# Kernel optimization log

Measured on AMD Instinct MI355X. Metric: run time of the kernel, lower is better.

## Reference

```python
import jax, jax.numpy as jnp
import numpy as np

HIDDEN = 1024
HEADS = 16
HEAD_DIM = HIDDEN // HEADS  # 64
B, S = 2, 2048


def setup_inputs() -> dict:
    key = jax.random.key(0)
    ks = jax.random.split(key, 12)
    lim_h = 1.0 / np.sqrt(HEAD_DIM)
    lim_o = 1.0 / np.sqrt(HIDDEN)
    u = lambda k, shape, lim: jax.random.uniform(k, shape, jnp.float32, -lim, lim)
    return {
        "query": jax.random.normal(ks[0], (B, S, HIDDEN), jnp.float32),
        "key": jax.random.normal(ks[1], (B, S, HIDDEN), jnp.float32),
        "value": jax.random.normal(ks[2], (B, S, HIDDEN), jnp.float32),
        "mask": jax.random.randint(ks[3], (B, 1, S, S), 0, 2, jnp.int32),
        "Wq": u(ks[4], (HEAD_DIM, HEAD_DIM), lim_h), "bq": u(ks[5], (HEAD_DIM,), lim_h),
        "Wk": u(ks[6], (HEAD_DIM, HEAD_DIM), lim_h), "bk": u(ks[7], (HEAD_DIM,), lim_h),
        "Wv": u(ks[8], (HEAD_DIM, HEAD_DIM), lim_h), "bv": u(ks[9], (HEAD_DIM,), lim_h),
        "Wo": u(ks[10], (HIDDEN, HIDDEN), lim_o), "bo": u(ks[11], (HIDDEN,), lim_o),
    }


def reference(query, key, value, mask, Wq, bq, Wk, bk, Wv, bv, Wo, bo):
    b = query.shape[0]
    # view [B, S, H, D]; per-head linear is SHARED across heads (head_dim x head_dim)
    q = query.reshape(b, -1, HEADS, HEAD_DIM) @ Wq.T + bq
    k = key.reshape(b, -1, HEADS, HEAD_DIM) @ Wk.T + bk
    v = value.reshape(b, -1, HEADS, HEAD_DIM) @ Wv.T + bv
    scores = jnp.einsum('nqhd,nkhd->nhqk', q, k)  # [B, H, Sq, Sk]
    scores = jnp.where(mask == 0, jnp.float32(-1e20), scores)
    # NOTE: original scales by sqrt(hidden_dim), not sqrt(head_dim)
    attn = jax.nn.softmax(scores / np.sqrt(HIDDEN).astype(np.float32), axis=3)
    out = jnp.einsum('nhql,nlhd->nqhd', attn, v).reshape(b, query.shape[1], HIDDEN)
    return out @ Wo.T + bo
```

## Files before the change

kernel.cpp:

```cpp
#include <hip/hip_runtime.h>
#include <hip/hip_bf16.h>

#define NB 2
#define NS 2048
#define NH 16
#define ND 64
#define NHID 1024

#define QSCALE 0.045084220f

typedef __attribute__((ext_vector_type(8))) short bf16x8;
typedef __attribute__((ext_vector_type(4))) short s16x4;
typedef __attribute__((ext_vector_type(4))) float f32x4;

typedef __attribute__((address_space(3))) unsigned int lds_u32;
typedef __attribute__((address_space(1))) unsigned int glb_u32;

__device__ inline void gl_lds16(const void* g, void* l) {
  __builtin_amdgcn_global_load_lds((const glb_u32*)g, (lds_u32*)l, 16, 0, 0);
}

__device__ inline short f2bf(float f) {
  __hip_bfloat16 h = __float2bfloat16(f);
  short s; __builtin_memcpy(&s, &h, 2); return s;
}

__device__ inline float selbit(float e, unsigned long long m) {
  float r;
  asm("v_cndmask_b32 %0, 0, %1, %2" : "=v"(r) : "v"(e), "s"(m));
  return r;
}

__device__ inline bf16x8 cvt8(const float* __restrict__ p) {
  float4 x = *(const float4*)p;
  float4 y = *(const float4*)(p + 4);
  bf16x8 r;
  r[0] = f2bf(x.x); r[1] = f2bf(x.y); r[2] = f2bf(x.z); r[3] = f2bf(x.w);
  r[4] = f2bf(y.x); r[5] = f2bf(y.y); r[6] = f2bf(y.z); r[7] = f2bf(y.w);
  return r;
}

__global__ __launch_bounds__(256) void prep(
    const int* __restrict__ mask, unsigned long long* __restrict__ mp,
    const float* __restrict__ Wq, const float* __restrict__ Wk,
    const float* __restrict__ Wv, const float* __restrict__ Wo,
    short* __restrict__ Wq_b, short* __restrict__ Wk_b,
    short* __restrict__ Wv_b, short* __restrict__ Wo_b)
{
  if (blockIdx.x < 512) {
    int idx = blockIdx.x * 256 + threadIdx.x;
    int lane = threadIdx.x & 63;
    int q4 = lane >> 4;
    int g4 = ((idx >> 6) << 4) | (lane & 15);
    int mt = g4 & 3, kt = (g4 >> 2) & 31, qg = (g4 >> 7) & 127, b = g4 >> 14;
    unsigned long long wq[4] = {0ull, 0ull, 0ull, 0ull};
#pragma unroll
    for (int cc = 0; cc < 4; ++cc) {
      int c2 = q4 * 4 + cc;
      const int4* p = (const int4*)(mask +
          ((size_t)(b * NS + qg * 16 + c2) * NS) + kt * 64 + mt * 16);
#pragma unroll
      for (int qq2 = 0; qq2 < 4; ++qq2) {
        int4 v = p[qq2];
        int sh = qq2 * 16 + c2;
        wq[0] |= (unsigned long long)(v.x != 0) << sh;
        wq[1] |= (unsigned long long)(v.y != 0) << sh;
        wq[2] |= (unsigned long long)(v.z != 0) << sh;
        wq[3] |= (unsigned long long)(v.w != 0) << sh;
      }
    }
#pragma unroll
    for (int r = 0; r < 4; ++r) {
      wq[r] |= __shfl_xor(wq[r], 16);
      wq[r] |= __shfl_xor(wq[r], 32);
    }
    mp[(size_t)g4 * 4 + q4] = wq[q4];
  } else {
    int i = ((blockIdx.x - 512) * 256 + threadIdx.x) * 4;
    const float* src; short* dst; int off; float sc = 1.0f;
    if (i < 1048576)      { src = Wo; dst = Wo_b; off = i; }
    else {
      int j = i - 1048576;
      if (j < 4096)       { src = Wq; dst = Wq_b; off = j; sc = QSCALE; }
      else if (j < 8192)  { src = Wk; dst = Wk_b; off = j - 4096; }
      else                { src = Wv; dst = Wv_b; off = j - 8192; }
    }
    float4 v = *(const float4*)(src + off);
    s16x4 o;
    o[0] = f2bf(v.x * sc); o[1] = f2bf(v.y * sc);
    o[2] = f2bf(v.z * sc); o[3] = f2bf(v.w * sc);
    *(s16x4*)(dst + off) = o;
  }
}

__global__ __launch_bounds__(256) void qkv_proj(
    const float* __restrict__ qin, const float* __restrict__ kin,
    const float* __restrict__ vin,
    const short* __restrict__ Wq_b, const float* __restrict__ bq,
    const short* __restrict__ Wk_b, const float* __restrict__ bk,
    const short* __restrict__ Wv_b, const float* __restrict__ bv,
    short* __restrict__ Qws, short* __restrict__ Kws, short* __restrict__ Vt)
{
  __shared__ __align__(16) short lds[4][16][72];
  const int tid = threadIdx.x;

  if (blockIdx.x < NB * NS / 4) {
    const int w = tid >> 6, lane = tid & 63;
    const int c = lane & 15, qq = lane >> 4;
    const int t = blockIdx.x * 4 + w;
    const int b = t >> 11, s = t & (NS - 1);
    const int aoff = (t * 16 + c) * 64 + qq * 8;
    const int row0 = lane >> 3, inner = lane & 7;

#pragma unroll
    for (int m = 0; m < 2; ++m) {
      const float* X  = (m == 0) ? qin  : kin;
      const short* W  = (m == 0) ? Wq_b : Wk_b;
      const float* bb = (m == 0) ? bq   : bk;
      short* dst      = (m == 0) ? Qws  : Kws;
      const float bsc = (m == 0) ? QSCALE : 1.0f;

      bf16x8 a0 = cvt8(X + aoff);
      bf16x8 a1 = cvt8(X + aoff + 32);

#pragma unroll
      for (int nt = 0; nt < 4; ++nt) {
        f32x4 z = {0.f, 0.f, 0.f, 0.f};
        const short* wp = W + (nt * 16 + c) * 64 + qq * 8;
        bf16x8 b0 = *(const bf16x8*)(wp);
        bf16x8 b1 = *(const bf16x8*)(wp + 32);
        z = __builtin_amdgcn_mfma_f32_16x16x32_bf16(a0, b0, z, 0, 0, 0);
        z = __builtin_amdgcn_mfma_f32_16x16x32_bf16(a1, b1, z, 0, 0, 0);
        float bias = bb[nt * 16 + c] * bsc;
#pragma unroll
        for (int r = 0; r < 4; ++r)
          lds[w][qq * 4 + r][nt * 16 + c] = f2bf(z[r] + bias);
      }

      bf16x8 v0 = *(const bf16x8*)&lds[w][row0][inner * 8];
      bf16x8 v1 = *(const bf16x8*)&lds[w][row0 + 8][inner * 8];
      int bh0 = b * NH + row0, bh1 = b * NH + row0 + 8;
      *(bf16x8*)(dst + (bh0 * NS + s) * 64 + inner * 8) = v0;
      *(bf16x8*)(dst + (bh1 * NS + s) * 64 + inner * 8) = v1;
    }
  } else {
    short (*ldsVT)[72] = (short (*)[72])lds;
    const int bid = blockIdx.x - NB * NS / 4;
    const int g = tid >> 6, lane = tid & 63;
    const int c = lane & 15, qq = lane >> 4;
    const int bh = bid >> 5;
    const int stile = bid & 31;
    const int b = bh >> 4, h = bh & 15;
    const int sb = stile * 64;

    bf16x8 wv[8];
    float bias[4];
#pragma unroll
    for (int nt = 0; nt < 4; ++nt) {
      const short* wp = Wv_b + (nt * 16 + c) * 64 + qq * 8;
      wv[nt * 2]     = *(const bf16x8*)(wp);
      wv[nt * 2 + 1] = *(const bf16x8*)(wp + 32);
      bias[nt] = bv[nt * 16 + c];
    }

    const float* ap = vin + ((size_t)((b * NS + sb + 16 * g + c) * 16 + h)) * 64 + qq * 8;
    bf16x8 a0 = cvt8(ap);
    bf16x8 a1 = cvt8(ap + 32);
#pragma unroll
    for (int nt = 0; nt < 4; ++nt) {
      f32x4 z = {0.f, 0.f, 0.f, 0.f};
      z = __builtin_amdgcn_mfma_f32_16x16x32_bf16(a0, wv[nt * 2], z, 0, 0, 0);
      z = __builtin_amdgcn_mfma_f32_16x16x32_bf16(a1, wv[nt * 2 + 1], z, 0, 0, 0);
      ushort4 u;
      u.x = (unsigned short)f2bf(z[0] + bias[nt]);
      u.y = (unsigned short)f2bf(z[1] + bias[nt]);
      u.z = (unsigned short)f2bf(z[2] + bias[nt]);
      u.w = (unsigned short)f2bf(z[3] + bias[nt]);
      *(ushort4*)&ldsVT[nt * 16 + c][16 * g + qq * 4] = u;
    }
    __syncthreads();

#pragma unroll
    for (int j = 0; j < 2; ++j) {
      int idx = tid + 256 * j;
      int d = idx >> 3, unit = idx & 7;
      bf16x8 o = *(const bf16x8*)&ldsVT[d][unit * 8];
      *(bf16x8*)(Vt + ((size_t)(bh * 64 + d)) * NS + sb + unit * 8) = o;
    }
  }
}

__global__ __launch_bounds__(256, 4) void attn(
    const short* __restrict__ Qws, const short* __restrict__ Kws,
    const short* __restrict__ Vt, const unsigned long long* __restrict__ Mp,
    short* __restrict__ AO)
{
  __shared__ __align__(16) short Ks[2][64][64];
  __shared__ __align__(16) short Vs[2][64][64];
  __shared__ __align__(16) short Ps[4][16][64];

  const int tid = threadIdx.x;
  const int w = tid >> 6, lane = tid & 63;
  const int c = lane & 15, qq = lane >> 4;
  const int bh = blockIdx.x & 31;
  const int qtile = blockIdx.x >> 5;
  const int b = bh >> 4, h = bh & 15;
  const int qbase = qtile * 64 + w * 16;
  const int ca2 = (lane & 7) << 1;

  const short* Qp = Qws + (size_t)bh * (NS * 64);
  const short* Kp = Kws + (size_t)bh * (NS * 64);
  const short* Vp = Vt + (size_t)bh * (64 * NS);

  const int wu = __builtin_amdgcn_readfirstlane(w);
  const unsigned long long* mbase =
      Mp + (size_t)(b * (NS / 16) + qtile * 4 + wu) * ((NS / 64) * 16);

  bf16x8 aq0, aq1;
  {
    const short* qp = Qp + (qbase + c) * 64 + qq * 8;
    aq0 = *(const bf16x8*)(qp);
    aq1 = *(const bf16x8*)(qp + 32);
  }

  float lsum = 0.f;
  f32x4 O[4];
#pragma unroll
  for (int dt = 0; dt < 4; ++dt) { f32x4 z = {0.f, 0.f, 0.f, 0.f}; O[dt] = z; }

  short* Pw = &Ps[w][c][0];

  const int srow = lane >> 3;
  const int sunit = (lane & 7) ^ srow;
  auto stage = [&](int kt, int buf) {
#pragma unroll
    for (int i = 0; i < 2; ++i) {
      int j = w * 2 + i;
      const short* gk = Kp + ((size_t)(kt * 64 + j * 8 + srow)) * 64 + sunit * 8;
      gl_lds16(gk, &Ks[buf][0][0] + j * 512);
      const short* gv = Vp + ((size_t)(j * 8 + srow)) * NS + kt * 64 + sunit * 8;
      gl_lds16(gv, &Vs[buf][0][0] + j * 512);
    }
  };

  stage(0, 0);
  __syncthreads();

  for (int kt = 0; kt < NS / 64; ++kt) {
    const int buf = kt & 1;
    if (kt < NS / 64 - 1) stage(kt + 1, buf ^ 1);

    unsigned long long mw[16];
#pragma unroll
    for (int i = 0; i < 16; ++i) mw[i] = mbase[(size_t)kt * 16 + i];

    f32x4 st[4];
    __builtin_amdgcn_s_setprio(1);
#pragma unroll
    for (int mt = 0; mt < 4; ++mt) {
      const short* kb = &Ks[buf][mt * 16 + c][0];
      bf16x8 ak0 = *(const bf16x8*)(kb + ((qq ^ (c & 7)) << 3));
      bf16x8 ak1 = *(const bf16x8*)(kb + (((4 + qq) ^ (c & 7)) << 3));
      f32x4 z = {0.f, 0.f, 0.f, 0.f};
      z = __builtin_amdgcn_mfma_f32_16x16x32_bf16(ak0, aq0, z, 0, 0, 0);
      z = __builtin_amdgcn_mfma_f32_16x16x32_bf16(ak1, aq1, z, 0, 0, 0);
      st[mt] = z;
    }
    __builtin_amdgcn_s_setprio(0);

#pragma unroll
    for (int mt = 0; mt < 4; ++mt) {
      f32x4 s = st[mt];
      float e0 = selbit(__builtin_amdgcn_exp2f(s[0]), mw[mt * 4 + 0]);
      float e1 = selbit(__builtin_amdgcn_exp2f(s[1]), mw[mt * 4 + 1]);
      float e2 = selbit(__builtin_amdgcn_exp2f(s[2]), mw[mt * 4 + 2]);
      float e3 = selbit(__builtin_amdgcn_exp2f(s[3]), mw[mt * 4 + 3]);
      lsum += (e0 + e1) + (e2 + e3);
      ushort4 u;
      u.x = (unsigned short)f2bf(e0);
      u.y = (unsigned short)f2bf(e1);
      u.z = (unsigned short)f2bf(e2);
      u.w = (unsigned short)f2bf(e3);
      *(ushort4*)&Pw[((mt * 4 + qq) ^ ca2) << 2] = u;
    }

    __builtin_amdgcn_s_setprio(1);
#pragma unroll
    for (int ks = 0; ks < 2; ++ks) {
      bf16x8 pf = *(const bf16x8*)&Pw[((ks * 8 + qq * 2) ^ ca2) << 2];
#pragma unroll
      for (int dt = 0; dt < 4; ++dt) {
        const short* vb = &Vs[buf][dt * 16 + c][0];
        bf16x8 vf = *(const bf16x8*)(vb + ((((ks << 2) + qq) ^ (c & 7)) << 3));
        O[dt] = __builtin_amdgcn_mfma_f32_16x16x32_bf16(vf, pf, O[dt], 0, 0, 0);
      }
    }
    __builtin_amdgcn_s_setprio(0);

    __syncthreads();
  }

  {
    float v = lsum;
    v += __shfl_xor(v, 16);
    v += __shfl_xor(v, 32);
    lsum = 1.0f / fmaxf(v, 1e-30f);
  }

  const int row = qbase + c;
#pragma unroll
  for (int dt = 0; dt < 4; ++dt) {
    ushort4 u;
    u.x = (unsigned short)f2bf(O[dt][0] * lsum);
    u.y = (unsigned short)f2bf(O[dt][1] * lsum);
    u.z = (unsigned short)f2bf(O[dt][2] * lsum);
    u.w = (unsigned short)f2bf(O[dt][3] * lsum);
    *(ushort4*)(AO + ((size_t)(b * NS + row)) * NHID + h * 64 + dt * 16 + qq * 4) = u;
  }
}

__global__ __launch_bounds__(256, 3) void oproj(
    const short* __restrict__ X, const short* __restrict__ Wo_b,
    const float* __restrict__ bo, float* __restrict__ out)
{
  __shared__ __align__(16) short As[2][64][64];
  __shared__ __align__(16) short Bs[2][128][64];
  const int tid = threadIdx.x;
  const int w = tid >> 6, lane = tid & 63;
  const int c = lane & 15, qq = lane >> 4;
  const int rowbase = blockIdx.x * 64;
  const int colbase = blockIdx.y * 128;
  const int mh = w & 1, nh = w >> 1;

  const int srow = lane >> 3;
  const int sunit = (lane & 7) ^ srow;

  auto stage = [&](int kb, int buf) {
#pragma unroll
    for (int i = 0; i < 6; ++i) {
      int t = w * 6 + i;
      if (t < 8) {
        const short* g = X + (size_t)(rowbase + t * 8 + srow) * NHID
                           + kb * 64 + sunit * 8;
        gl_lds16(g, &As[buf][0][0] + t * 512);
      } else {
        int j = t - 8;
        const short* g = Wo_b + (size_t)(colbase + j * 8 + srow) * NHID
                              + kb * 64 + sunit * 8;
        gl_lds16(g, &Bs[buf][0][0] + j * 512);
      }
    }
  };

  f32x4 acc[2][4];
#pragma unroll
  for (int mt = 0; mt < 2; ++mt)
#pragma unroll
    for (int nt = 0; nt < 4; ++nt) { f32x4 z = {0.f, 0.f, 0.f, 0.f}; acc[mt][nt] = z; }

  stage(0, 0);
  __syncthreads();

  for (int kb = 0; kb < NHID / 64; ++kb) {
    const int buf = kb & 1;
    if (kb < NHID / 64 - 1) stage(kb + 1, buf ^ 1);

    bf16x8 af[2][2];
#pragma unroll
    for (int mt = 0; mt < 2; ++mt) {
      const short* ap = &As[buf][mh * 32 + mt * 16 + c][0];
#pragma unroll
      for (int ks = 0; ks < 2; ++ks)
        af[mt][ks] = *(const bf16x8*)(ap + ((((ks << 2) + qq) ^ (c & 7)) << 3));
    }
#pragma unroll
    for (int nt = 0; nt < 4; ++nt) {
      const short* bp = &Bs[buf][nh * 64 + nt * 16 + c][0];
#pragma unroll
      for (int ks = 0; ks < 2; ++ks) {
        bf16x8 bf = *(const bf16x8*)(bp + ((((ks << 2) + qq) ^ (c & 7)) << 3));
#pragma unroll
        for (int mt = 0; mt < 2; ++mt)
          acc[mt][nt] = __builtin_amdgcn_mfma_f32_16x16x32_bf16(af[mt][ks], bf, acc[mt][nt], 0, 0, 0);
      }
    }

    __syncthreads();
  }

#pragma unroll
  for (int nt = 0; nt < 4; ++nt) {
    int col = colbase + nh * 64 + nt * 16 + c;
    float bias = bo[col];
#pragma unroll
    for (int mt = 0; mt < 2; ++mt) {
      int row = rowbase + mh * 32 + mt * 16 + qq * 4;
#pragma unroll
      for (int r = 0; r < 4; ++r)
        out[(size_t)(row + r) * NHID + col] = acc[mt][nt][r] + bias;
    }
  }
}

extern "C" void kernel_launch(void* const* d_in, const int* in_sizes, int n_in,
                              void* d_out, int out_size, void* d_ws, size_t ws_size,
                              hipStream_t stream) {
  const float* qin = (const float*)d_in[0];
  const float* kin = (const float*)d_in[1];
  const float* vin = (const float*)d_in[2];
  const int*  mask = (const int*)d_in[3];
  const float* Wq = (const float*)d_in[4];
  const float* bq = (const float*)d_in[5];
  const float* Wk = (const float*)d_in[6];
  const float* bk = (const float*)d_in[7];
  const float* Wv = (const float*)d_in[8];
  const float* bv = (const float*)d_in[9];
  const float* Wo = (const float*)d_in[10];
  const float* bo = (const float*)d_in[11];
  float* out = (float*)d_out;

  char* ws = (char*)d_ws;
  short* Qws = (short*)(ws);
  short* Kws = (short*)(ws + (size_t)(8 << 20));
  short* Vt  = (short*)(ws + (size_t)(16 << 20));
  short* AO  = (short*)(ws + (size_t)(24 << 20));
  unsigned long long* Mp = (unsigned long long*)(ws + (size_t)(32 << 20));
  short* Wo_b = (short*)(ws + (size_t)(33 << 20));
  short* Wq_b = (short*)(ws + (size_t)(35 << 20));
  short* Wk_b = (short*)(ws + (size_t)(35 << 20) + 8192);
  short* Wv_b = (short*)(ws + (size_t)(35 << 20) + 16384);

  prep<<<1548, 256, 0, stream>>>(mask, Mp, Wq, Wk, Wv, Wo, Wq_b, Wk_b, Wv_b, Wo_b);
  qkv_proj<<<NB * NS / 4 + (NB * NH) * (NS / 64), 256, 0, stream>>>(
      qin, kin, vin, Wq_b, bq, Wk_b, bk, Wv_b, bv, Qws, Kws, Vt);
  attn<<<(NB * NH) * (NS / 64), 256, 0, stream>>>(Qws, Kws, Vt, Mp, AO);
  oproj<<<dim3(64, 8), 256, 0, stream>>>(AO, Wo_b, bo, out);
}
```

Measured before the change: 210.4 us.

## Process two 16-row query tiles per wave in attention kernel

Each wave now handles 32 query rows instead of 16, so the attention block covers 128 queries and the grid halves. Every K/V tile staged into LDS and every K/V fragment read feeds twice as many MFMAs, which halves global K/V traffic and the LDS reads per query. In exchange, register pressure roughly doubles (launch bounds lowered from 4 to 2 blocks per CU), the P buffer in LDS doubles, and the grid drops to 512 blocks, which may cut occupancy and latency hiding.

```diff
diff --git a/kernel.cpp b/kernel.cpp
--- a/kernel.cpp
+++ b/kernel.cpp
@@ -190,14 +190,14 @@
   }
 }
 
-__global__ __launch_bounds__(256, 4) void attn(
+__global__ __launch_bounds__(256, 2) void attn(
     const short* __restrict__ Qws, const short* __restrict__ Kws,
     const short* __restrict__ Vt, const unsigned long long* __restrict__ Mp,
     short* __restrict__ AO)
 {
   __shared__ __align__(16) short Ks[2][64][64];
   __shared__ __align__(16) short Vs[2][64][64];
-  __shared__ __align__(16) short Ps[4][16][64];
+  __shared__ __align__(16) short Ps[4][32][64];
 
   const int tid = threadIdx.x;
   const int w = tid >> 6, lane = tid & 63;
@@ -205,7 +205,7 @@
   const int bh = blockIdx.x & 31;
   const int qtile = blockIdx.x >> 5;
   const int b = bh >> 4, h = bh & 15;
-  const int qbase = qtile * 64 + w * 16;
+  const int qbase = qtile * 128 + w * 32;
   const int ca2 = (lane & 7) << 1;
 
   const short* Qp = Qws + (size_t)bh * (NS * 64);
@@ -213,22 +213,24 @@
   const short* Vp = Vt + (size_t)bh * (64 * NS);
 
   const int wu = __builtin_amdgcn_readfirstlane(w);
-  const unsigned long long* mbase =
-      Mp + (size_t)(b * (NS / 16) + qtile * 4 + wu) * ((NS / 64) * 16);
-
-  bf16x8 aq0, aq1;
-  {
-    const short* qp = Qp + (qbase + c) * 64 + qq * 8;
-    aq0 = *(const bf16x8*)(qp);
-    aq1 = *(const bf16x8*)(qp + 32);
-  }
-
-  float lsum = 0.f;
-  f32x4 O[4];
-#pragma unroll
-  for (int dt = 0; dt < 4; ++dt) { f32x4 z = {0.f, 0.f, 0.f, 0.f}; O[dt] = z; }
-
-  short* Pw = &Ps[w][c][0];
+  const unsigned long long* mbase0 =
+      Mp + (size_t)(b * (NS / 16) + qtile * 8 + wu * 2) * ((NS / 64) * 16);
+  const unsigned long long* mbase1 = mbase0 + ((NS / 64) * 16);
+
+  bf16x8 aq[2][2];
+#pragma unroll
+  for (int nq = 0; nq < 2; ++nq) {
+    const short* qp = Qp + (qbase + nq * 16 + c) * 64 + qq * 8;
+    aq[nq][0] = *(const bf16x8*)(qp);
+    aq[nq][1] = *(const bf16x8*)(qp + 32);
+  }
+
+  float lsum[2] = {0.f, 0.f};
+  f32x4 O[2][4];
+#pragma unroll
+  for (int nq = 0; nq < 2; ++nq)
+#pragma unroll
+    for (int dt = 0; dt < 4; ++dt) { f32x4 z = {0.f, 0.f, 0.f, 0.f}; O[nq][dt] = z; }
 
   const int srow = lane >> 3;
   const int sunit = (lane & 7) ^ srow;
@@ -250,49 +252,61 @@
     const int buf = kt & 1;
     if (kt < NS / 64 - 1) stage(kt + 1, buf ^ 1);
 
-    unsigned long long mw[16];
-#pragma unroll
-    for (int i = 0; i < 16; ++i) mw[i] = mbase[(size_t)kt * 16 + i];
-
-    f32x4 st[4];
+    f32x4 st[4][2];
     __builtin_amdgcn_s_setprio(1);
 #pragma unroll
     for (int mt = 0; mt < 4; ++mt) {
       const short* kb = &Ks[buf][mt * 16 + c][0];
       bf16x8 ak0 = *(const bf16x8*)(kb + ((qq ^ (c & 7)) << 3));
       bf16x8 ak1 = *(const bf16x8*)(kb + (((4 + qq) ^ (c & 7)) << 3));
-      f32x4 z = {0.f, 0.f, 0.f, 0.f};
-      z = __builtin_amdgcn_mfma_f32_16x16x32_bf16(ak0, aq0, z, 0, 0, 0);
-      z = __builtin_amdgcn_mfma_f32_16x16x32_bf16(ak1, aq1, z, 0, 0, 0);
-      st[mt] = z;
+#pragma unroll
+      for (int nq = 0; nq < 2; ++nq) {
+        f32x4 z = {0.f, 0.f, 0.f, 0.f};
+        z = __builtin_amdgcn_mfma_f32_16x16x32_bf16(ak0, aq[nq][0], z, 0, 0, 0);
+        z = __builtin_amdgcn_mfma_f32_16x16x32_bf16(ak1, aq[nq][1], z, 0, 0, 0);
+        st[mt][nq] = z;
+      }
     }
     __builtin_amdgcn_s_setprio(0);
 
 #pragma unroll
-    for (int mt = 0; mt < 4; ++mt) {
-      f32x4 s = st[mt];
-      float e0 = selbit(__builtin_amdgcn_exp2f(s[0]), mw[mt * 4 + 0]);
-      float e1 = selbit(__builtin_amdgcn_exp2f(s[1]), mw[mt * 4 + 1]);
-      float e2 = selbit(__builtin_amdgcn_exp2f(s[2]), mw[mt * 4 + 2]);
-      float e3 = selbit(__builtin_amdgcn_exp2f(s[3]), mw[mt * 4 + 3]);
-      lsum += (e0 + e1) + (e2 + e3);
-      ushort4 u;
-      u.x = (unsigned short)f2bf(e0);
-      u.y = (unsigned short)f2bf(e1);
-      u.z = (unsigned short)f2bf(e2);
-      u.w = (unsigned short)f2bf(e3);
-      *(ushort4*)&Pw[((mt * 4 + qq) ^ ca2) << 2] = u;
+    for (int nq = 0; nq < 2; ++nq) {
+      const unsigned long long* mb = (nq == 0) ? mbase0 : mbase1;
+      unsigned long long mw[16];
+#pragma unroll
+      for (int i = 0; i < 16; ++i) mw[i] = mb[(size_t)kt * 16 + i];
+      short* Pw = &Ps[w][nq * 16 + c][0];
+#pragma unroll
+      for (int mt = 0; mt < 4; ++mt) {
+        f32x4 s = st[mt][nq];
+        float e0 = selbit(__builtin_amdgcn_exp2f(s[0]), mw[mt * 4 + 0]);
+        float e1 = selbit(__builtin_amdgcn_exp2f(s[1]), mw[mt * 4 + 1]);
+        float e2 = selbit(__builtin_amdgcn_exp2f(s[2]), mw[mt * 4 + 2]);
+        float e3 = selbit(__builtin_amdgcn_exp2f(s[3]), mw[mt * 4 + 3]);
+        lsum[nq] += (e0 + e1) + (e2 + e3);
+        ushort4 u;
+        u.x = (unsigned short)f2bf(e0);
+        u.y = (unsigned short)f2bf(e1);
+        u.z = (unsigned short)f2bf(e2);
+        u.w = (unsigned short)f2bf(e3);
+        *(ushort4*)&Pw[((mt * 4 + qq) ^ ca2) << 2] = u;
+      }
     }
 
     __builtin_amdgcn_s_setprio(1);
 #pragma unroll
     for (int ks = 0; ks < 2; ++ks) {
-      bf16x8 pf = *(const bf16x8*)&Pw[((ks * 8 + qq * 2) ^ ca2) << 2];
+      bf16x8 pf[2];
+#pragma unroll
+      for (int nq = 0; nq < 2; ++nq)
+        pf[nq] = *(const bf16x8*)&Ps[w][nq * 16 + c][((ks * 8 + qq * 2) ^ ca2) << 2];
 #pragma unroll
       for (int dt = 0; dt < 4; ++dt) {
         const short* vb = &Vs[buf][dt * 16 + c][0];
         bf16x8 vf = *(const bf16x8*)(vb + ((((ks << 2) + qq) ^ (c & 7)) << 3));
-        O[dt] = __builtin_amdgcn_mfma_f32_16x16x32_bf16(vf, pf, O[dt], 0, 0, 0);
+#pragma unroll
+        for (int nq = 0; nq < 2; ++nq)
+          O[nq][dt] = __builtin_amdgcn_mfma_f32_16x16x32_bf16(vf, pf[nq], O[nq][dt], 0, 0, 0);
       }
     }
     __builtin_amdgcn_s_setprio(0);
@@ -300,22 +314,26 @@
     __syncthreads();
   }
 
-  {
-    float v = lsum;
+#pragma unroll
+  for (int nq = 0; nq < 2; ++nq) {
+    float v = lsum[nq];
     v += __shfl_xor(v, 16);
     v += __shfl_xor(v, 32);
-    lsum = 1.0f / fmaxf(v, 1e-30f);
-  }
-
-  const int row = qbase + c;
-#pragma unroll
-  for (int dt = 0; dt < 4; ++dt) {
-    ushort4 u;
-    u.x = (unsigned short)f2bf(O[dt][0] * lsum);
-    u.y = (unsigned short)f2bf(O[dt][1] * lsum);
-    u.z = (unsigned short)f2bf(O[dt][2] * lsum);
-    u.w = (unsigned short)f2bf(O[dt][3] * lsum);
-    *(ushort4*)(AO + ((size_t)(b * NS + row)) * NHID + h * 64 + dt * 16 + qq * 4) = u;
+    lsum[nq] = 1.0f / fmaxf(v, 1e-30f);
+  }
+
+#pragma unroll
+  for (int nq = 0; nq < 2; ++nq) {
+    int row = qbase + nq * 16 + c;
+#pragma unroll
+    for (int dt = 0; dt < 4; ++dt) {
+      ushort4 u;
+      u.x = (unsigned short)f2bf(O[nq][dt][0] * lsum[nq]);
+      u.y = (unsigned short)f2bf(O[nq][dt][1] * lsum[nq]);
+      u.z = (unsigned short)f2bf(O[nq][dt][2] * lsum[nq]);
+      u.w = (unsigned short)f2bf(O[nq][dt][3] * lsum[nq]);
+      *(ushort4*)(AO + ((size_t)(b * NS + row)) * NHID + h * 64 + dt * 16 + qq * 4) = u;
+    }
   }
 }
 
@@ -433,6 +451,6 @@
   prep<<<1548, 256, 0, stream>>>(mask, Mp, Wq, Wk, Wv, Wo, Wq_b, Wk_b, Wv_b, Wo_b);
   qkv_proj<<<NB * NS / 4 + (NB * NH) * (NS / 64), 256, 0, stream>>>(
       qin, kin, vin, Wq_b, bq, Wk_b, bk, Wv_b, bv, Qws, Kws, Vt);
-  attn<<<(NB * NH) * (NS / 64), 256, 0, stream>>>(Qws, Kws, Vt, Mp, AO);
+  attn<<<(NB * NH) * (NS / 128), 256, 0, stream>>>(Qws, Kws, Vt, Mp, AO);
   oproj<<<dim3(64, 8), 256, 0, stream>>>(AO, Wo_b, bo, out);
 }
```

After: 206.7 us. No clear change (-1.7%).
